# Kernel optimization log

Measured on AMD Instinct MI355X. Metric: run time of the kernel, lower is better.

Reference implementation:

```python
import jax, jax.numpy as jnp
import numpy as np

B, C, H, W = 8, 64, 112, 112
F, KH, KW = 128, 3, 3
SPARSITY = 0.7  # fraction of kernel entries zeroed (Uniform connector)


def setup_inputs() -> dict:
    key = jax.random.key(0)
    k1, k2, k3 = jax.random.split(key, 3)
    inputs = jax.random.normal(k1, (B, C, H, W), dtype=jnp.float32)
    fan_in = C * KH * KW
    limit = float(np.sqrt(6.0 / (F + fan_in)))
    vals = jax.random.uniform(k2, (F, fan_in), minval=-limit, maxval=limit, dtype=jnp.float32)
    mask = (jax.random.uniform(k3, (F, fan_in)) >= SPARSITY).astype(jnp.float32)
    kernel = vals * mask  # dense representation of the sparse kernel
    return {"inputs": inputs, "kernel": kernel}


def _extract_patches(x, kh, kw):
    # x: [B, S1, S2, C]; VALID padding, stride 1, rate 1.
    # Matches tf.image.extract_patches depth ordering: (pi, pj) major, channel minor.
    Bb, S1, S2, Cc = x.shape
    o1, o2 = S1 - kh + 1, S2 - kw + 1
    pats = jnp.stack(
        [x[:, i:i + o1, j:j + o2, :] for i in range(kh) for j in range(kw)],
        axis=3,
    )  # [B, o1, o2, kh*kw, C]
    return pats.reshape(Bb, o1, o2, kh * kw * Cc)


def reference(inputs, kernel):
    # inputs: [B, C, H, W] (NCHW, per bias_add data_format and build())
    x = jnp.transpose(inputs, (0, 3, 2, 1))  # [B, W, H, C] (perm [0,3,2,1] in original)
    p = _extract_patches(x, KH, KW)          # [B, oW, oH, KH*KW*C]
    # spmm(kernel [F, K], im2col [K, B*oW*oH]) expressed as a single contraction
    out = jnp.einsum('bwhk,fk->bfwh', p, kernel)  # [B, F, oW, oH]
    return out
```

## Files before the change

### kernel.cpp

```cpp
#include <hip/hip_runtime.h>

typedef unsigned short u16;
typedef unsigned int u32;
typedef _Float16 f16x8 __attribute__((ext_vector_type(8)));
typedef float f32x4 __attribute__((ext_vector_type(4)));

#define B_ 8
#define C_ 64
#define H_ 112
#define W_ 112
#define HW_ 12544
#define F_ 128
#define OH_ 110
#define OW_ 110
#define NPOS 96800
#define KK_ 576
#define NWG 757
#define OCTSTRIDE 802816

__device__ __forceinline__ void gl_lds16(const void* g, void* l) {
  __builtin_amdgcn_global_load_lds((const __attribute__((address_space(1))) void*)g,
                                   (__attribute__((address_space(3))) void*)l,
                                   16, 0, 0);
}

__global__ __launch_bounds__(256) void prep_inputT(const float* __restrict__ in,
                                                   u16* __restrict__ xT) {
  __shared__ float tile[8][8][113];
  const int bid = blockIdx.x;
  const int b = bid / 112;
  const int r = bid % 112;
  const int oct = r / 14;
  const int hs = (r % 14) * 8;
  const int tid = threadIdx.x;

  for (int idx = tid; idx < 8 * 8 * 112; idx += 256) {
    int c = idx / 896;
    int rem = idx - c * 896;
    int h = rem / 112;
    int w = rem - h * 112;
    tile[c][h][w] = in[(((size_t)(b * 64 + oct * 8 + c)) * 112 + (hs + h)) * 112 + w];
  }
  __syncthreads();

  for (int idx = tid; idx < 896; idx += 256) {
    int w = idx >> 3;
    int h = idx & 7;
    f16x8 v;
#pragma unroll
    for (int c = 0; c < 8; ++c) v[c] = (_Float16)tile[c][h][w];
    size_t o = ((((size_t)oct * B_ + b) * W_ + w) * H_ + (hs + h)) * 8;
    *(f16x8*)(xT + o) = v;
  }
}

__global__ __launch_bounds__(256) void prep_ker(const float* __restrict__ k,
                                                u16* __restrict__ kT) {
  int idx = blockIdx.x * 256 + threadIdx.x;
  if (idx < F_ * KK_) {
    _Float16 h = (_Float16)k[idx];
    kT[idx] = __builtin_bit_cast(u16, h);
  }
}

__global__ __launch_bounds__(256, 4) void conv_mfma(
    const u16* __restrict__ xT, const u16* __restrict__ kT,
    float* __restrict__ out) {
  __shared__ u16 lds[2][128 * 32];

  const int tid = threadIdx.x;
  const int wave = tid >> 6;
  const int lane = tid & 63;

  const int orig = blockIdx.x;
  const int xcd = orig & 7;
  const int sub = orig >> 3;
  const int wg = (xcd < 5 ? xcd * 95 : 475 + (xcd - 5) * 94) + sub;
  const int n0 = wg * 128;

  const int l15 = lane & 15;
  const int l4 = lane >> 4;
  const int wr = wave >> 1;
  const int wc = wave & 1;

  const int rlo = lane >> 2;
  const int q = (lane & 3) ^ ((lane >> 3) & 3);
  int aOff[2];
#pragma unroll
  for (int it = 0; it < 2; ++it) {
    int row = (it * 4 + wave) * 16 + rlo;
    aOff[it] = row * KK_ + q * 8;
  }

  int posOff[4];
#pragma unroll
  for (int ni = 0; ni < 4; ++ni) {
    int n = n0 + wc * 64 + ni * 16 + l15;
    if (n >= NPOS) n = 0;
    int b = n / (OW_ * OH_);
    int r = n - b * (OW_ * OH_);
    int w = r / OH_;
    int h = r - w * OH_;
    posOff[ni] = ((b * W_ + w) * H_ + h) * 8;
  }
  const int l4Off = l4 * OCTSTRIDE;

  f32x4 acc[4][4] = {};

  auto stageA = [&](int s, int d) {
    const int tap = s >> 1;
    const int half = s & 1;
    const int offA = tap * C_ + half * 32;
#pragma unroll
    for (int it = 0; it < 2; ++it) {
      const u32 dst = (u32)((it * 4 + wave) * 1024);
      gl_lds16(kT + aOff[it] + offA, (char*)&lds[d][0] + dst);
    }
  };

  stageA(0, 0);
  __syncthreads();

  for (int s = 0; s < 18; ++s) {
    const int cur = s & 1;
    const int tap = s >> 1;
    const int half = s & 1;
    const int i = tap / 3;
    const int j = tap - i * 3;
    const int sShift = (i * H_ + j) * 8 + half * 4 * OCTSTRIDE;

    f16x8 bh[4];
#pragma unroll
    for (int ni = 0; ni < 4; ++ni) {
      bh[ni] = *(const f16x8*)(xT + posOff[ni] + l4Off + sShift);
    }

    if (s < 17) stageA(s + 1, cur ^ 1);

    f16x8 ah[4];
#pragma unroll
    for (int mi = 0; mi < 4; ++mi) {
      int row = wr * 64 + mi * 16 + l15;
      int e = row * 32 + ((l4 ^ ((row >> 1) & 3)) * 8);
      ah[mi] = *(const f16x8*)&lds[cur][e];
    }

#pragma unroll
    for (int mi = 0; mi < 4; ++mi)
#pragma unroll
      for (int ni = 0; ni < 4; ++ni) {
        acc[mi][ni] = __builtin_amdgcn_mfma_f32_16x16x32_f16(ah[mi], bh[ni], acc[mi][ni], 0, 0, 0);
      }

    __syncthreads();
  }

#pragma unroll
  for (int ni = 0; ni < 4; ++ni) {
    int n = n0 + wc * 64 + ni * 16 + l15;
    if (n >= NPOS) continue;
    int b = n / (OW_ * OH_);
    int r = n - b * (OW_ * OH_);
    int w = r / OH_;
    int h = r - w * OH_;
    float* op = out + ((size_t)(b * F_) * OW_ + w) * OH_ + h;
#pragma unroll
    for (int mi = 0; mi < 4; ++mi) {
      int fbase = wr * 64 + mi * 16 + l4 * 4;
#pragma unroll
      for (int qq = 0; qq < 4; ++qq) {
        op[(size_t)(fbase + qq) * (OW_ * OH_)] = acc[mi][ni][qq];
      }
    }
  }
}

__global__ void naive_conv(const float* __restrict__ in, const float* __restrict__ ker,
                           float* __restrict__ out) {
  int idx = blockIdx.x * 256 + threadIdx.x;
  const int total = B_ * F_ * OW_ * OH_;
  if (idx >= total) return;
  int h = idx % OH_;
  int w = (idx / OH_) % OW_;
  int f = (idx / (OW_ * OH_)) % F_;
  int b = idx / (F_ * OW_ * OH_);
  float s = 0.f;
  for (int tap = 0; tap < 9; ++tap) {
    int i = tap / 3, j = tap % 3;
    const float* ip = in + ((size_t)b * C_ * H_ + (h + j)) * W_ + (w + i);
    const float* kp = ker + (size_t)f * KK_ + tap * C_;
    for (int c = 0; c < C_; ++c) s += ip[(size_t)c * HW_] * kp[c];
  }
  out[idx] = s;
}

extern "C" void kernel_launch(void* const* d_in, const int* in_sizes, int n_in,
                              void* d_out, int out_size, void* d_ws, size_t ws_size,
                              hipStream_t stream) {
  const float* in = (const float*)d_in[0];
  const float* ker = (const float*)d_in[1];
  float* out = (float*)d_out;

  const size_t xElems = (size_t)B_ * H_ * W_ * C_;
  const size_t kElems = (size_t)F_ * KK_;
  const size_t need = (xElems + kElems) * 2;

  if (ws_size < need) {
    int total = B_ * F_ * OW_ * OH_;
    naive_conv<<<(total + 255) / 256, 256, 0, stream>>>(in, ker, out);
    return;
  }

  u16* xT = (u16*)d_ws;
  u16* kT = xT + xElems;

  prep_inputT<<<896, 256, 0, stream>>>(in, xT);
  prep_ker<<<(int)((kElems + 255) / 256), 256, 0, stream>>>(ker, kT);
  conv_mfma<<<NWG, 256, 0, stream>>>(xT, kT, out);
}
```

Baseline: 43.68 us.

## Load whole fp16 kernel into LDS once and drop per-step double buffering

The kernel weights are pre-laid-out in k-octet-major order so each workgroup can copy the full 128x576 fp16 weight matrix (144 KB) into LDS in one bulk pass. The 18-step loop then reads A fragments straight from LDS with no per-step staging or barriers, and the first B load is hoisted ahead of the bulk copy. The cost is 144 KB of LDS per workgroup, which limits occupancy to one block per CU, and a larger fill before any MFMA work can start.

```diff
diff --git a/kernel.cpp b/kernel.cpp
--- a/kernel.cpp
+++ b/kernel.cpp
@@ -17,6 +17,7 @@
 #define KK_ 576
 #define NWG 757
 #define OCTSTRIDE 802816
+#define AELEMS 73728
 
 __device__ __forceinline__ void gl_lds16(const void* g, void* l) {
   __builtin_amdgcn_global_load_lds((const __attribute__((address_space(1))) void*)g,
@@ -54,19 +55,23 @@
   }
 }
 
-__global__ __launch_bounds__(256) void prep_ker(const float* __restrict__ k,
-                                                u16* __restrict__ kT) {
+__global__ __launch_bounds__(256) void prep_kerT(const float* __restrict__ k,
+                                                 u16* __restrict__ kT) {
   int idx = blockIdx.x * 256 + threadIdx.x;
-  if (idx < F_ * KK_) {
-    _Float16 h = (_Float16)k[idx];
+  if (idx < AELEMS) {
+    int ko = idx >> 10;
+    int rem = idx & 1023;
+    int f = rem >> 3;
+    int c = rem & 7;
+    _Float16 h = (_Float16)k[f * KK_ + ko * 8 + c];
     kT[idx] = __builtin_bit_cast(u16, h);
   }
 }
 
-__global__ __launch_bounds__(256, 4) void conv_mfma(
+__global__ __launch_bounds__(256, 1) void conv_mfma(
     const u16* __restrict__ xT, const u16* __restrict__ kT,
     float* __restrict__ out) {
-  __shared__ u16 lds[2][128 * 32];
+  __shared__ u16 lds[AELEMS];
 
   const int tid = threadIdx.x;
   const int wave = tid >> 6;
@@ -82,15 +87,6 @@
   const int l4 = lane >> 4;
   const int wr = wave >> 1;
   const int wc = wave & 1;
-
-  const int rlo = lane >> 2;
-  const int q = (lane & 3) ^ ((lane >> 3) & 3);
-  int aOff[2];
-#pragma unroll
-  for (int it = 0; it < 2; ++it) {
-    int row = (it * 4 + wave) * 16 + rlo;
-    aOff[it] = row * KK_ + q * 8;
-  }
 
   int posOff[4];
 #pragma unroll
@@ -105,24 +101,21 @@
   }
   const int l4Off = l4 * OCTSTRIDE;
 
+  f16x8 b0[4];
+#pragma unroll
+  for (int ni = 0; ni < 4; ++ni) b0[ni] = *(const f16x8*)(xT + posOff[ni] + l4Off);
+
+#pragma unroll
+  for (int it = 0; it < 36; ++it) {
+    const u32 off = (u32)((it * 256 + tid) * 16);
+    gl_lds16((const char*)kT + off, (char*)lds + off);
+  }
+  __syncthreads();
+
   f32x4 acc[4][4] = {};
 
-  auto stageA = [&](int s, int d) {
-    const int tap = s >> 1;
-    const int half = s & 1;
-    const int offA = tap * C_ + half * 32;
-#pragma unroll
-    for (int it = 0; it < 2; ++it) {
-      const u32 dst = (u32)((it * 4 + wave) * 1024);
-      gl_lds16(kT + aOff[it] + offA, (char*)&lds[d][0] + dst);
-    }
-  };
-
-  stageA(0, 0);
-  __syncthreads();
-
+#pragma unroll
   for (int s = 0; s < 18; ++s) {
-    const int cur = s & 1;
     const int tap = s >> 1;
     const int half = s & 1;
     const int i = tap / 3;
@@ -130,29 +123,25 @@
     const int sShift = (i * H_ + j) * 8 + half * 4 * OCTSTRIDE;
 
     f16x8 bh[4];
-#pragma unroll
-    for (int ni = 0; ni < 4; ++ni) {
-      bh[ni] = *(const f16x8*)(xT + posOff[ni] + l4Off + sShift);
+    if (s == 0) {
+#pragma unroll
+      for (int ni = 0; ni < 4; ++ni) bh[ni] = b0[ni];
+    } else {
+#pragma unroll
+      for (int ni = 0; ni < 4; ++ni)
+        bh[ni] = *(const f16x8*)(xT + posOff[ni] + l4Off + sShift);
     }
 
-    if (s < 17) stageA(s + 1, cur ^ 1);
-
     f16x8 ah[4];
-#pragma unroll
-    for (int mi = 0; mi < 4; ++mi) {
-      int row = wr * 64 + mi * 16 + l15;
-      int e = row * 32 + ((l4 ^ ((row >> 1) & 3)) * 8);
-      ah[mi] = *(const f16x8*)&lds[cur][e];
-    }
+    const int aBase = ((s * 4 + l4) * 128 + wr * 64 + l15) * 8;
+#pragma unroll
+    for (int mi = 0; mi < 4; ++mi) ah[mi] = *(const f16x8*)&lds[aBase + mi * 128];
 
 #pragma unroll
     for (int mi = 0; mi < 4; ++mi)
 #pragma unroll
-      for (int ni = 0; ni < 4; ++ni) {
+      for (int ni = 0; ni < 4; ++ni)
         acc[mi][ni] = __builtin_amdgcn_mfma_f32_16x16x32_f16(ah[mi], bh[ni], acc[mi][ni], 0, 0, 0);
-      }
-
-    __syncthreads();
   }
 
 #pragma unroll
@@ -202,8 +191,7 @@
   float* out = (float*)d_out;
 
   const size_t xElems = (size_t)B_ * H_ * W_ * C_;
-  const size_t kElems = (size_t)F_ * KK_;
-  const size_t need = (xElems + kElems) * 2;
+  const size_t need = (xElems + AELEMS) * 2;
 
   if (ws_size < need) {
     int total = B_ * F_ * OW_ * OH_;
@@ -215,6 +203,6 @@
   u16* kT = xT + xElems;
 
   prep_inputT<<<896, 256, 0, stream>>>(in, xT);
-  prep_ker<<<(int)((kElems + 255) / 256), 256, 0, stream>>>(ker, kT);
+  prep_kerT<<<(int)((AELEMS + 255) / 256), 256, 0, stream>>>(ker, kT);
   conv_mfma<<<NWG, 256, 0, stream>>>(xT, kT, out);
 }
```

Result: slower. 46.48 us (+6.4%).
